# Kernel tuning notes

Measured on AMD Instinct MI355X. Metric: run time of the kernel, lower is better.

Reference implementation:

```python
import jax, jax.numpy as jnp
import numpy as np

N_POINTS = 8192
D_FEAT = 256
WEIGHT = 1.0  # self.weight
EPS = 1e-12


def _pairwise_dist(x):
    # Euclidean pairwise distances, [N, N]
    sq = jnp.sum(x * x, axis=-1)
    d2 = sq[:, None] + sq[None, :] - 2.0 * (x @ x.T)
    d2 = jnp.maximum(d2, 0.0)
    return jnp.sqrt(d2 + EPS)


def _mst_edge_weights(dist):
    # Prim's algorithm, vectorized O(N^2). The MST edge lengths are exactly
    # the death times of the H0 (dim-0) persistence diagram of the
    # Vietoris-Rips filtration (all births = 0). jit-compatible via lax.scan.
    n = dist.shape[0]
    big = jnp.asarray(1e30, dist.dtype)
    in_tree0 = jnp.zeros((n,), dtype=bool).at[0].set(True)
    mindist0 = dist[0]

    def step(carry, _):
        in_tree, mindist = carry
        masked = jnp.where(in_tree, big, mindist)
        j = jnp.argmin(masked)
        w = masked[j]                      # weight of MST edge added this step
        in_tree = in_tree.at[j].set(True)
        mindist = jnp.minimum(mindist, dist[j])
        return (in_tree, mindist), w

    _, weights = jax.lax.scan(step, (in_tree0, mindist0), None, length=n - 1)
    return weights  # [N-1] H0 death times


def _persistent_entropy(lifetimes):
    # PersistentEntropy.compute: p_i = l_i / sum(l); E = -sum p_i log p_i
    total = jnp.sum(lifetimes)
    p = lifetimes / (total + EPS)
    return -jnp.sum(p * jnp.log(p + EPS))


def setup_inputs() -> dict:
    key = jax.random.key(0)
    representations = jax.random.normal(key, (N_POINTS, D_FEAT), dtype=jnp.float32)
    return {"representations": representations}


def reference(representations):
    # PersistentHomology.compute_from_distance: VR filtration over the point
    # cloud; H0 diagram computed exactly via MST (single-linkage). Higher
    # dims (dim=1) are not produced, so the `if dim < len(diagrams)` guard
    # skips them, matching GPU PH implementations that emit H0 only.
    dist = _pairwise_dist(representations)
    deaths = _mst_edge_weights(dist)
    entropy = _persistent_entropy(deaths)
    loss = -entropy  # target_entropy is None -> maximize entropy
    return WEIGHT * loss
```

## Files before the change

kernel.cpp:

```cpp
#include <hip/hip_runtime.h>
#include <hip/hip_bf16.h>
#include <hip/hip_fp16.h>

#define NP 8192
#define DF 256
#define NROUNDS 13
#define CAND_K 48
#define NBINS 2048

typedef unsigned long long u64;
typedef unsigned int u32;
typedef unsigned short u16;
using bf16x8 = __attribute__((ext_vector_type(8))) short;
using f32x4  = __attribute__((ext_vector_type(4))) float;
using u16x8  = __attribute__((ext_vector_type(8))) u16;

__device__ __forceinline__ u16 f2bf(float f) {
  __hip_bfloat16 h = __float2bfloat16(f);
  return __builtin_bit_cast(u16, h);
}
__device__ __forceinline__ u16 f2h_bits(float f) {
  _Float16 h = (_Float16)f;
  return __builtin_bit_cast(u16, h);
}


__global__ void init_kernel(int* comp, u64* compmin, int* edgeCnt, int* nComps) {
  int i = blockIdx.x * 256 + threadIdx.x;
  if (i < NP) { comp[i] = i; compmin[i] = ~0ull; }
  if (i == 0) { *edgeCnt = 0; *nComps = NP; }
}


__global__ __launch_bounds__(64) void sq_kernel(const float* __restrict__ X, float* __restrict__ sq) {
  int i = blockIdx.x;
  float4 v = ((const float4*)(X + (size_t)i * DF))[threadIdx.x];
  float s = v.x * v.x + v.y * v.y + v.z * v.z + v.w * v.w;
#pragma unroll
  for (int off = 32; off >= 1; off >>= 1) s += __shfl_down(s, off);
  if (threadIdx.x == 0) sq[i] = s;
}


__global__ __launch_bounds__(256) void cvt_kernel(const float* __restrict__ X, u16* __restrict__ Xb) {
  int idx = (blockIdx.x * 256 + threadIdx.x) * 8;
  float4 a = ((const float4*)(X + idx))[0];
  float4 b = ((const float4*)(X + idx))[1];
  u16x8 o;
  o[0] = f2bf(a.x); o[1] = f2bf(a.y); o[2] = f2bf(a.z); o[3] = f2bf(a.w);
  o[4] = f2bf(b.x); o[5] = f2bf(b.y); o[6] = f2bf(b.z); o[7] = f2bf(b.w);
  *(u16x8*)(Xb + idx) = o;
}


template <bool PRE>
__global__ __launch_bounds__(256) void build_dist_kernel(
    const float* __restrict__ X, const u16* __restrict__ Xb,
    const float* __restrict__ sq, _Float16* __restrict__ d2) {
  __shared__ __align__(16) u16 smem[128 * 144];
  u16* At = smem;
  u16* Bt = smem + 128 * 40;
  const int t = threadIdx.x;
  const int m0 = blockIdx.y * 128, n0 = blockIdx.x * 128;
  const int wid = t >> 6, lane = t & 63;
  const int wm = wid >> 1, wn = wid & 1;
  const int lrow = lane & 15, lk = lane >> 4;
  f32x4 acc[4][4] = {};

  const int srow = t >> 1, shalf = t & 1;
  for (int k0 = 0; k0 < DF; k0 += 32) {
    u16x8 av0, av1, bv0, bv1;
    if (PRE) {
      const u16* pa = Xb + (size_t)(m0 + srow) * DF + k0 + shalf * 16;
      av0 = *(const u16x8*)pa; av1 = *(const u16x8*)(pa + 8);
      const u16* pb = Xb + (size_t)(n0 + srow) * DF + k0 + shalf * 16;
      bv0 = *(const u16x8*)pb; bv1 = *(const u16x8*)(pb + 8);
    } else {
      const float4* pa = (const float4*)(X + (size_t)(m0 + srow) * DF + k0 + shalf * 16);
      float4 a0 = pa[0], a1 = pa[1], a2 = pa[2], a3 = pa[3];
      av0[0]=f2bf(a0.x); av0[1]=f2bf(a0.y); av0[2]=f2bf(a0.z); av0[3]=f2bf(a0.w);
      av0[4]=f2bf(a1.x); av0[5]=f2bf(a1.y); av0[6]=f2bf(a1.z); av0[7]=f2bf(a1.w);
      av1[0]=f2bf(a2.x); av1[1]=f2bf(a2.y); av1[2]=f2bf(a2.z); av1[3]=f2bf(a2.w);
      av1[4]=f2bf(a3.x); av1[5]=f2bf(a3.y); av1[6]=f2bf(a3.z); av1[7]=f2bf(a3.w);
      const float4* pb = (const float4*)(X + (size_t)(n0 + srow) * DF + k0 + shalf * 16);
      float4 b0 = pb[0], b1 = pb[1], b2 = pb[2], b3 = pb[3];
      bv0[0]=f2bf(b0.x); bv0[1]=f2bf(b0.y); bv0[2]=f2bf(b0.z); bv0[3]=f2bf(b0.w);
      bv0[4]=f2bf(b1.x); bv0[5]=f2bf(b1.y); bv0[6]=f2bf(b1.z); bv0[7]=f2bf(b1.w);
      bv1[0]=f2bf(b2.x); bv1[1]=f2bf(b2.y); bv1[2]=f2bf(b2.z); bv1[3]=f2bf(b2.w);
      bv1[4]=f2bf(b3.x); bv1[5]=f2bf(b3.y); bv1[6]=f2bf(b3.z); bv1[7]=f2bf(b3.w);
    }
    __syncthreads();
    *(u16x8*)&At[srow * 40 + shalf * 16] = av0;
    *(u16x8*)&At[srow * 40 + shalf * 16 + 8] = av1;
    *(u16x8*)&Bt[srow * 40 + shalf * 16] = bv0;
    *(u16x8*)&Bt[srow * 40 + shalf * 16 + 8] = bv1;
    __syncthreads();
    bf16x8 af[4], bfr[4];
#pragma unroll
    for (int fm = 0; fm < 4; ++fm)
      af[fm] = *(const bf16x8*)&At[(wm * 64 + fm * 16 + lrow) * 40 + lk * 8];
#pragma unroll
    for (int fn = 0; fn < 4; ++fn)
      bfr[fn] = *(const bf16x8*)&Bt[(wn * 64 + fn * 16 + lrow) * 40 + lk * 8];
#pragma unroll
    for (int fm = 0; fm < 4; ++fm)
#pragma unroll
      for (int fn = 0; fn < 4; ++fn)
        acc[fm][fn] = __builtin_amdgcn_mfma_f32_16x16x32_bf16(af[fm], bfr[fn], acc[fm][fn], 0, 0, 0);
  }
  __syncthreads();

  float sqj[4];
#pragma unroll
  for (int fn = 0; fn < 4; ++fn) sqj[fn] = sq[n0 + wn * 64 + fn * 16 + lrow];
#pragma unroll
  for (int fm = 0; fm < 4; ++fm) {
#pragma unroll
    for (int r = 0; r < 4; ++r) {
      int row = wm * 64 + fm * 16 + lk * 4 + r;
      int i = m0 + row;
      float si = sq[i];
#pragma unroll
      for (int fn = 0; fn < 4; ++fn) {
        int col = wn * 64 + fn * 16 + lrow;
        float dd = si + sqj[fn] - 2.0f * acc[fm][fn][r];
        dd = fmaxf(dd, 0.0f);
        if (i == n0 + col) dd = INFINITY;
        smem[row * 144 + col] = f2h_bits(dd);
      }
    }
  }
  __syncthreads();
#pragma unroll
  for (int k = 0; k < 8; ++k) {
    int flat = k * 256 + t;
    int row = flat >> 4, cb = (flat & 15) * 8;
    *(u16x8*)&d2[(size_t)(m0 + row) * NP + n0 + cb] = *(const u16x8*)&smem[row * 144 + cb];
  }
}


__global__ __launch_bounds__(256) void topk_kernel(const _Float16* __restrict__ d2,
                                                   u64* __restrict__ candT,
                                                   u32* __restrict__ candCnt) {
  __shared__ u16 rowbuf[NP];
  __shared__ u32 hist[NBINS];
  __shared__ u32 scanw[4];
  __shared__ int swred[4];
  __shared__ int sB;
  __shared__ u32 sCnt;
  const int i = blockIdx.x;
  const int t = threadIdx.x;
  const u16* row = (const u16*)(d2 + (size_t)i * NP);
  for (int b = t; b < NBINS; b += 256) hist[b] = 0;
  if (t == 0) sCnt = 0;
  __syncthreads();
  for (int base = t * 8; base < NP; base += 2048) {
    u16x8 v = *(const u16x8*)(row + base);
    *(u16x8*)&rowbuf[base] = v;
#pragma unroll
    for (int q = 0; q < 8; ++q) atomicAdd(&hist[v[q] >> 5], 1u);
  }
  __syncthreads();
  u32 loc[8]; u32 s = 0;
#pragma unroll
  for (int q = 0; q < 8; ++q) { loc[q] = hist[t * 8 + q]; s += loc[q]; }
  u32 pre = s;
  for (int off = 1; off < 64; off <<= 1) {
    u32 o = __shfl_up(pre, off);
    if ((t & 63) >= off) pre += o;
  }
  if ((t & 63) == 63) scanw[t >> 6] = pre;
  __syncthreads();
  u32 wbase = 0;
  for (int w = 0; w < (t >> 6); ++w) wbase += scanw[w];
  u32 c = wbase + pre - s;
  int lb = -1;
#pragma unroll
  for (int q = 0; q < 8; ++q) {
    c += loc[q];
    if (c >= 1 && c <= CAND_K) lb = t * 8 + q;
  }
#pragma unroll
  for (int off = 32; off >= 1; off >>= 1) {
    int o = __shfl_down(lb, off);
    lb = lb > o ? lb : o;
  }
  if ((t & 63) == 0) swred[t >> 6] = lb;
  __syncthreads();
  if (t == 0) {
    int m = swred[0];
#pragma unroll
    for (int w = 1; w < 4; ++w) m = m > swred[w] ? m : swred[w];
    sB = m;
  }
  __syncthreads();
  const int B = sB;
  if (B >= 0) {
    for (int base = t * 8; base < NP; base += 2048) {
#pragma unroll
      for (int q = 0; q < 8; ++q) {
        u16 v = rowbuf[base + q];
        if ((int)(v >> 5) <= B) {
          u32 pos = atomicAdd(&sCnt, 1u);
          if (pos < CAND_K) {
            int j = base + q;
            int lo = i < j ? i : j;
            int hi = i ^ j ^ lo;
            candT[(size_t)pos * NP + i] = ((u64)v << 26) | ((u64)lo << 13) | (u64)hi;
          }
        }
      }
    }
  }
  __syncthreads();
  if (t == 0) {
    u32 n = sCnt;
    candCnt[i] = (n == 0 || n > CAND_K) ? 0x80000000u : n;
  }
}


__global__ __launch_bounds__(256) void round_min_kernel(
    const _Float16* __restrict__ d2, const u64* __restrict__ candT,
    const u32* __restrict__ candCnt, const int* __restrict__ comp,
    u64* __restrict__ compmin, const int* __restrict__ nComps) {
  if (*nComps == 1) return;
  __shared__ int fbl[256];
  __shared__ int fbn;
  __shared__ u64 sred[4];
  const int t = threadIdx.x;
  const int i = blockIdx.x * 256 + t;
  if (t == 0) fbn = 0;
  __syncthreads();
  const int ci = comp[i];
  u32 cc = candCnt[i];
  int n = (int)(cc & 0x7fffffffu);
  u64 best = ~0ull;
  for (int k = 0; k < n; ++k) {
    u64 key = candT[(size_t)k * NP + i];
    int lo = (int)((key >> 13) & 0x1FFF);
    int hi = (int)(key & 0x1FFF);
    int j = (lo == i) ? hi : lo;
    if (comp[j] != ci && key < best) best = key;
  }
  if (best != ~0ull && !(cc & 0x80000000u)) {
    atomicMin(&compmin[ci], best);
  } else {
    int p = atomicAdd(&fbn, 1);
    fbl[p] = i;
  }
  __syncthreads();
  for (int f = 0; f < fbn; ++f) {
    int r = fbl[f];
    int cr = comp[r];
    const u16* rowp = (const u16*)(d2 + (size_t)r * NP);
    u64 b2 = ~0ull;
    for (int base = t * 8; base < NP; base += 2048) {
      u16x8 v = *(const u16x8*)(rowp + base);
      int4 c0 = *(const int4*)(comp + base);
      int4 c1 = *(const int4*)(comp + base + 4);
      int cs[8] = {c0.x, c0.y, c0.z, c0.w, c1.x, c1.y, c1.z, c1.w};
#pragma unroll
      for (int q = 0; q < 8; ++q) {
        if (cs[q] != cr) {
          int j = base + q;
          int lo = r < j ? r : j;
          int hi = r ^ j ^ lo;
          u64 k = ((u64)v[q] << 26) | ((u64)lo << 13) | (u64)hi;
          b2 = k < b2 ? k : b2;
        }
      }
    }
#pragma unroll
    for (int off = 32; off >= 1; off >>= 1) {
      u64 o = __shfl_down(b2, off);
      b2 = b2 < o ? b2 : o;
    }
    if ((t & 63) == 0) sred[t >> 6] = b2;
    __syncthreads();
    if (t == 0) {
      b2 = sred[0];
#pragma unroll
      for (int w = 1; w < 4; ++w) b2 = b2 < sred[w] ? b2 : sred[w];
      if (b2 != ~0ull) atomicMin(&compmin[cr], b2);
    }
    __syncthreads();
  }
}


__global__ void select_kernel(const float* __restrict__ X, const float* __restrict__ sq,
                              const int* __restrict__ comp, const u64* __restrict__ compmin,
                              int* __restrict__ parent, float* __restrict__ edgeW,
                              int* __restrict__ edgeCnt, const int* __restrict__ nComps) {
  int c = blockIdx.x * blockDim.x + threadIdx.x;
  if (c >= NP) return;
  if (*nComps == 1) { parent[c] = c; return; }
  u64 m = compmin[c];
  if (m == ~0ull) { parent[c] = c; return; }
  int a = (int)((m >> 13) & 0x1FFF);
  int b = (int)(m & 0x1FFF);
  int j = (comp[a] == c) ? b : a;
  int d = comp[j];
  bool mutual = false;
  u64 md = compmin[d];
  if (md != ~0ull) {
    int a2 = (int)((md >> 13) & 0x1FFF);
    int b2 = (int)(md & 0x1FFF);
    int j2 = (comp[a2] == d) ? b2 : a2;
    mutual = (comp[j2] == c);
  }
  if (mutual && c > d) { parent[c] = d; return; }
  parent[c] = mutual ? c : d;
  const float4* pa = (const float4*)(X + (size_t)a * DF);
  const float4* pb = (const float4*)(X + (size_t)b * DF);
  float dot = 0.f;
#pragma unroll 8
  for (int k = 0; k < DF / 4; ++k) {
    float4 va = pa[k], vb = pb[k];
    dot += va.x * vb.x + va.y * vb.y + va.z * vb.z + va.w * vb.w;
  }
  float dd = sq[a] + sq[b] - 2.f * dot;
  float w = sqrtf(fmaxf(dd, 0.f) + 1e-12f);
  int idx = atomicAdd(edgeCnt, 1);
  if (idx < NP) edgeW[idx] = w;
}


__global__ __launch_bounds__(1024) void jump_relabel_kernel(
    const int* __restrict__ parent, int* __restrict__ comp,
    u64* __restrict__ compmin, int* __restrict__ nComps) {
  if (*nComps == 1) return;
  __shared__ int sp[NP];
  __shared__ unsigned char fl[NP];
  __shared__ int scnt;
  __shared__ int sch;
  const int t = threadIdx.x;
  for (int c = t; c < NP; c += 1024) { sp[c] = parent[c]; fl[c] = 0; }
  if (t == 0) { scnt = 0; sch = 0; }
  __syncthreads();
  for (int it = 0; it < NROUNDS; ++it) {
    int ch = 0;
    for (int c = t; c < NP; c += 1024) {
      int p = sp[c];
      int pp = sp[p];
      if (p != pp) { sp[c] = pp; ch = 1; }
    }
    if (ch) sch = 1;
    __syncthreads();
    if (!sch) break;
    __syncthreads();
    if (t == 0) sch = 0;
    __syncthreads();
  }
  int part = 0;
  for (int i = t; i < NP; i += 1024) {
    int nc = sp[comp[i]];
    comp[i] = nc;
    fl[nc] = 1;
  }
  __syncthreads();
  for (int c = t; c < NP; c += 1024) part += fl[c];
#pragma unroll
  for (int off = 32; off >= 1; off >>= 1) part += __shfl_down(part, off);
  if ((t & 63) == 0) atomicAdd(&scnt, part);
  for (int c = t; c < NP; c += 1024) compmin[c] = ~0ull;
  __syncthreads();
  if (t == 0) *nComps = scnt;
}


__global__ __launch_bounds__(1024) void entropy_kernel(const float* __restrict__ edgeW,
                                                       const int* __restrict__ edgeCnt,
                                                       float* __restrict__ out) {
  __shared__ float sred[16];
  __shared__ float stot;
  int ne = *edgeCnt;
  if (ne > NP) ne = NP;
  float s = 0.f;
  for (int k = threadIdx.x; k < ne; k += 1024) s += edgeW[k];
#pragma unroll
  for (int off = 32; off >= 1; off >>= 1) s += __shfl_down(s, off);
  int lane = threadIdx.x & 63, wv = threadIdx.x >> 6;
  if (lane == 0) sred[wv] = s;
  __syncthreads();
  if (threadIdx.x == 0) {
    float tt = 0.f;
#pragma unroll
    for (int w = 0; w < 16; ++w) tt += sred[w];
    stot = tt;
  }
  __syncthreads();
  float total = stot;
  float acc = 0.f;
  for (int k = threadIdx.x; k < ne; k += 1024) {
    float p = edgeW[k] / (total + 1e-12f);
    acc += p * logf(p + 1e-12f);
  }
#pragma unroll
  for (int off = 32; off >= 1; off >>= 1) acc += __shfl_down(acc, off);
  if (lane == 0) sred[wv] = acc;
  __syncthreads();
  if (threadIdx.x == 0) {
    float tt = 0.f;
#pragma unroll
    for (int w = 0; w < 16; ++w) tt += sred[w];
    out[0] = tt;
  }
}


extern "C" void kernel_launch(void* const* d_in, const int* in_sizes, int n_in,
                              void* d_out, int out_size, void* d_ws, size_t ws_size,
                              hipStream_t stream) {
  const float* X = (const float*)d_in[0];
  float* out = (float*)d_out;
  char* ws = (char*)d_ws;

  const size_t nn = (size_t)NP * NP;
  size_t off = (nn * 2 + 255) & ~(size_t)255;
  _Float16* d2 = (_Float16*)ws;
  float* sq = (float*)(ws + off);      off += (size_t)NP * 4;
  int* comp = (int*)(ws + off);        off += (size_t)NP * 4;
  u64* compmin = (u64*)(ws + off);     off += (size_t)NP * 8;
  int* parent = (int*)(ws + off);      off += (size_t)NP * 4;
  float* edgeW = (float*)(ws + off);   off += (size_t)NP * 4;
  u32* candCnt = (u32*)(ws + off);     off += (size_t)NP * 4;
  int* edgeCnt = (int*)(ws + off);     off += 64;
  int* nComps = (int*)(ws + off);      off += 64;
  off = (off + 255) & ~(size_t)255;
  u16* Xb = (u16*)(ws + off);
  u64* candT = (u64*)(ws + off);
  const bool PRE = (ws_size >= off + (size_t)NP * DF * 2);

  init_kernel<<<NP / 256, 256, 0, stream>>>(comp, compmin, edgeCnt, nComps);
  sq_kernel<<<NP, 64, 0, stream>>>(X, sq);
  if (PRE) {
    cvt_kernel<<<NP * DF / (256 * 8), 256, 0, stream>>>(X, Xb);
    build_dist_kernel<true><<<dim3(NP / 128, NP / 128), 256, 0, stream>>>(X, Xb, sq, d2);
  } else {
    build_dist_kernel<false><<<dim3(NP / 128, NP / 128), 256, 0, stream>>>(X, Xb, sq, d2);
  }
  topk_kernel<<<NP, 256, 0, stream>>>(d2, candT, candCnt);
  for (int r = 0; r < NROUNDS; ++r) {
    round_min_kernel<<<NP / 256, 256, 0, stream>>>(d2, candT, candCnt, comp, compmin, nComps);
    select_kernel<<<NP / 256, 256, 0, stream>>>(X, sq, comp, compmin, parent, edgeW, edgeCnt, nComps);
    jump_relabel_kernel<<<1, 1024, 0, stream>>>(parent, comp, compmin, nComps);
  }
  entropy_kernel<<<1, 1024, 0, stream>>>(edgeW, edgeCnt, out);
}
```

Before: 428.4 us.

## Contract graph to dense component matrix after early Boruvka rounds

Splits the Boruvka MST into two phases. After a few rounds over candidate lists, components are densely relabeled and one pass over the full distance matrix builds a component-by-component min-edge matrix (NC=512). The remaining rounds then run on that small matrix instead of rescanning rows. Fallback row scans also move out of a per-block serial loop into a separate grid-wide kernel. The design assumes at most 512 components remain after four rounds; if more remain, the dense ids overflow and the result is wrong.

```diff
diff --git a/kernel.cpp b/kernel.cpp
--- a/kernel.cpp
+++ b/kernel.cpp
@@ -4,9 +4,12 @@
 
 #define NP 8192
 #define DF 256
-#define NROUNDS 13
+#define PH1 4
+#define PH2 9
+#define NC 512
 #define CAND_K 48
 #define NBINS 2048
+#define ALLR 13
 
 typedef unsigned long long u64;
 typedef unsigned int u32;
@@ -23,11 +26,17 @@
   _Float16 h = (_Float16)f;
   return __builtin_bit_cast(u16, h);
 }
-
-
-__global__ void init_kernel(int* comp, u64* compmin, int* edgeCnt, int* nComps) {
+__device__ __forceinline__ u64 mkkey(u32 vbits, int i, int j) {
+  int lo = i < j ? i : j;
+  int hi = i ^ j ^ lo;
+  return ((u64)vbits << 26) | ((u64)lo << 13) | (u64)hi;
+}
+
+
+__global__ void init_kernel(int* comp, u64* compmin, int* edgeCnt, int* nComps, int* fbCnt) {
   int i = blockIdx.x * 256 + threadIdx.x;
   if (i < NP) { comp[i] = i; compmin[i] = ~0ull; }
+  if (blockIdx.x == 0 && threadIdx.x < 16) fbCnt[threadIdx.x] = 0;
   if (i == 0) { *edgeCnt = 0; *nComps = NP; }
 }
 
@@ -203,12 +212,7 @@
         u16 v = rowbuf[base + q];
         if ((int)(v >> 5) <= B) {
           u32 pos = atomicAdd(&sCnt, 1u);
-          if (pos < CAND_K) {
-            int j = base + q;
-            int lo = i < j ? i : j;
-            int hi = i ^ j ^ lo;
-            candT[(size_t)pos * NP + i] = ((u64)v << 26) | ((u64)lo << 13) | (u64)hi;
-          }
+          if (pos < CAND_K) candT[(size_t)pos * NP + i] = mkkey(v, i, base + q);
         }
       }
     }
@@ -221,18 +225,13 @@
 }
 
 
-__global__ __launch_bounds__(256) void round_min_kernel(
-    const _Float16* __restrict__ d2, const u64* __restrict__ candT,
-    const u32* __restrict__ candCnt, const int* __restrict__ comp,
-    u64* __restrict__ compmin, const int* __restrict__ nComps) {
+__global__ __launch_bounds__(256) void cand_min_kernel(
+    const u64* __restrict__ candT, const u32* __restrict__ candCnt,
+    const int* __restrict__ comp, u64* __restrict__ compmin,
+    const int* __restrict__ nComps, int* __restrict__ fbList,
+    int* __restrict__ fbCnt, int r) {
   if (*nComps == 1) return;
-  __shared__ int fbl[256];
-  __shared__ int fbn;
-  __shared__ u64 sred[4];
-  const int t = threadIdx.x;
-  const int i = blockIdx.x * 256 + t;
-  if (t == 0) fbn = 0;
-  __syncthreads();
+  const int i = blockIdx.x * 256 + threadIdx.x;
   const int ci = comp[i];
   u32 cc = candCnt[i];
   int n = (int)(cc & 0x7fffffffu);
@@ -247,43 +246,50 @@
   if (best != ~0ull && !(cc & 0x80000000u)) {
     atomicMin(&compmin[ci], best);
   } else {
-    int p = atomicAdd(&fbn, 1);
-    fbl[p] = i;
-  }
-  __syncthreads();
-  for (int f = 0; f < fbn; ++f) {
-    int r = fbl[f];
-    int cr = comp[r];
-    const u16* rowp = (const u16*)(d2 + (size_t)r * NP);
-    u64 b2 = ~0ull;
+    int p = atomicAdd(&fbCnt[r], 1);
+    fbList[p] = i;
+  }
+}
+
+
+__global__ __launch_bounds__(256) void fb_kernel(
+    const _Float16* __restrict__ d2, const int* __restrict__ comp,
+    u64* __restrict__ compmin, const int* __restrict__ fbList,
+    const int* __restrict__ fbCnt, int r, const int* __restrict__ nComps) {
+  if (*nComps == 1) return;
+  __shared__ u64 sred[4];
+  const int t = threadIdx.x;
+  const int n = fbCnt[r];
+  for (int idx = blockIdx.x; idx < n; idx += gridDim.x) {
+    const int i = fbList[idx];
+    const int ci = comp[i];
+    const u16* row = (const u16*)(d2 + (size_t)i * NP);
+    u64 best = ~0ull;
     for (int base = t * 8; base < NP; base += 2048) {
-      u16x8 v = *(const u16x8*)(rowp + base);
+      u16x8 v = *(const u16x8*)(row + base);
       int4 c0 = *(const int4*)(comp + base);
       int4 c1 = *(const int4*)(comp + base + 4);
       int cs[8] = {c0.x, c0.y, c0.z, c0.w, c1.x, c1.y, c1.z, c1.w};
 #pragma unroll
       for (int q = 0; q < 8; ++q) {
-        if (cs[q] != cr) {
-          int j = base + q;
-          int lo = r < j ? r : j;
-          int hi = r ^ j ^ lo;
-          u64 k = ((u64)v[q] << 26) | ((u64)lo << 13) | (u64)hi;
-          b2 = k < b2 ? k : b2;
+        if (cs[q] != ci) {
+          u64 k = mkkey(v[q], i, base + q);
+          best = k < best ? k : best;
         }
       }
     }
 #pragma unroll
     for (int off = 32; off >= 1; off >>= 1) {
-      u64 o = __shfl_down(b2, off);
-      b2 = b2 < o ? b2 : o;
-    }
-    if ((t & 63) == 0) sred[t >> 6] = b2;
+      u64 o = __shfl_down(best, off);
+      best = best < o ? best : o;
+    }
+    if ((t & 63) == 0) sred[t >> 6] = best;
     __syncthreads();
     if (t == 0) {
-      b2 = sred[0];
-#pragma unroll
-      for (int w = 1; w < 4; ++w) b2 = b2 < sred[w] ? b2 : sred[w];
-      if (b2 != ~0ull) atomicMin(&compmin[cr], b2);
+      best = sred[0];
+#pragma unroll
+      for (int w = 1; w < 4; ++w) best = best < sred[w] ? best : sred[w];
+      if (best != ~0ull) atomicMin(&compmin[ci], best);
     }
     __syncthreads();
   }
@@ -328,19 +334,24 @@
 }
 
 
+template <bool DENSE>
 __global__ __launch_bounds__(1024) void jump_relabel_kernel(
     const int* __restrict__ parent, int* __restrict__ comp,
-    u64* __restrict__ compmin, int* __restrict__ nComps) {
+    u64* __restrict__ compmin, int* __restrict__ nComps,
+    u16* __restrict__ dcomp, int* __restrict__ comp2, int* __restrict__ parent2,
+    u64* __restrict__ compmin2, int* __restrict__ ncDense) {
   if (*nComps == 1) return;
   __shared__ int sp[NP];
-  __shared__ unsigned char fl[NP];
+  __shared__ u16 did[NP];
+  __shared__ int swsum[16];
   __shared__ int scnt;
   __shared__ int sch;
   const int t = threadIdx.x;
-  for (int c = t; c < NP; c += 1024) { sp[c] = parent[c]; fl[c] = 0; }
+  const int lane = t & 63, wv = t >> 6;
+  for (int c = t; c < NP; c += 1024) { sp[c] = parent[c]; did[c] = 0; }
   if (t == 0) { scnt = 0; sch = 0; }
   __syncthreads();
-  for (int it = 0; it < NROUNDS; ++it) {
+  for (int it = 0; it < 13; ++it) {
     int ch = 0;
     for (int c = t; c < NP; c += 1024) {
       int p = sp[c];
@@ -354,18 +365,183 @@
     if (t == 0) sch = 0;
     __syncthreads();
   }
-  int part = 0;
   for (int i = t; i < NP; i += 1024) {
     int nc = sp[comp[i]];
     comp[i] = nc;
-    fl[nc] = 1;
-  }
-  __syncthreads();
-  for (int c = t; c < NP; c += 1024) part += fl[c];
+    did[nc] = 1;
+  }
+  __syncthreads();
+  if constexpr (!DENSE) {
+    int part = 0;
+    for (int c = t; c < NP; c += 1024) part += did[c];
+#pragma unroll
+    for (int off = 32; off >= 1; off >>= 1) part += __shfl_down(part, off);
+    if (lane == 0) atomicAdd(&scnt, part);
+    for (int c = t; c < NP; c += 1024) compmin[c] = ~0ull;
+    __syncthreads();
+    if (t == 0) *nComps = scnt;
+  } else {
+    int f[8]; int s = 0;
+#pragma unroll
+    for (int q = 0; q < 8; ++q) { f[q] = did[t * 8 + q]; s += f[q]; }
+    int incl = s;
+    for (int off = 1; off < 64; off <<= 1) {
+      int o = __shfl_up(incl, off);
+      if (lane >= off) incl += o;
+    }
+    if (lane == 63) swsum[wv] = incl;
+    __syncthreads();
+    int wbase = 0;
+    for (int w = 0; w < wv; ++w) wbase += swsum[w];
+    int e = wbase + incl - s;
+#pragma unroll
+    for (int q = 0; q < 8; ++q) {
+      if (f[q]) { did[t * 8 + q] = (u16)e; ++e; }
+    }
+    __syncthreads();
+    for (int i = t; i < NP; i += 1024) dcomp[i] = did[comp[i]];
+    if (t < NC) { comp2[t] = t; parent2[t] = t; compmin2[t] = ~0ull; }
+    if (t == 0) {
+      int total = 0;
+#pragma unroll
+      for (int w = 0; w < 16; ++w) total += swsum[w];
+      *nComps = total;
+      *ncDense = total;
+    }
+  }
+}
+
+
+__global__ __launch_bounds__(256) void minit_kernel(u64* __restrict__ M) {
+  int idx = (blockIdx.x * 256 + threadIdx.x) * 4;
+#pragma unroll
+  for (int q = 0; q < 4; ++q) M[idx + q] = ~0ull;
+}
+
+
+__global__ __launch_bounds__(256) void contract_kernel(
+    const _Float16* __restrict__ d2, const u16* __restrict__ dcomp,
+    u64* __restrict__ M) {
+  __shared__ u32 table[NC];
+  const int i = blockIdx.x;
+  const int t = threadIdx.x;
+  for (int b = t; b < NC; b += 256) table[b] = ~0u;
+  __syncthreads();
+  const int ci = dcomp[i];
+  const u16* row = (const u16*)(d2 + (size_t)i * NP);
+  for (int base = t * 8; base < NP; base += 2048) {
+    u16x8 v = *(const u16x8*)(row + base);
+    u16x8 cj = *(const u16x8*)(dcomp + base);
+#pragma unroll
+    for (int q = 0; q < 8; ++q) {
+      if (cj[q] != ci) {
+        u32 k32 = ((u32)v[q] << 13) | (u32)(base + q);
+        atomicMin(&table[cj[q]], k32);
+      }
+    }
+  }
+  __syncthreads();
+  for (int b = t; b < NC; b += 256) {
+    u32 k32 = table[b];
+    if (k32 != ~0u) {
+      u64 key = mkkey(k32 >> 13, i, (int)(k32 & 0x1FFF));
+      u64* addr = &M[(size_t)ci * NC + b];
+      if (key < *addr) atomicMin(addr, key);
+    }
+  }
+}
+
+
+__global__ __launch_bounds__(64) void rmin2_kernel(const u64* __restrict__ M,
+                                                   const int* __restrict__ comp2,
+                                                   u64* __restrict__ compmin2,
+                                                   const int* __restrict__ nComps) {
+  if (*nComps == 1) return;
+  const int a = blockIdx.x;
+  const int t = threadIdx.x;
+  const int ca = comp2[a];
+  u64 best = ~0ull;
+  for (int b = t; b < NC; b += 64) {
+    u64 k = M[(size_t)a * NC + b];
+    if (k != ~0ull && comp2[b] != ca && k < best) best = k;
+  }
+#pragma unroll
+  for (int off = 32; off >= 1; off >>= 1) {
+    u64 o = __shfl_down(best, off);
+    best = best < o ? best : o;
+  }
+  if (t == 0 && best != ~0ull) atomicMin(&compmin2[ca], best);
+}
+
+
+__global__ void select2_kernel(const float* __restrict__ X, const float* __restrict__ sq,
+                               const u16* __restrict__ dcomp, const int* __restrict__ comp2,
+                               const u64* __restrict__ compmin2, int* __restrict__ parent2,
+                               float* __restrict__ edgeW, int* __restrict__ edgeCnt,
+                               const int* __restrict__ nComps) {
+  int c = blockIdx.x * blockDim.x + threadIdx.x;
+  if (c >= NC) return;
+  if (*nComps == 1) { parent2[c] = c; return; }
+  u64 m = compmin2[c];
+  if (m == ~0ull) { parent2[c] = c; return; }
+  int a = (int)((m >> 13) & 0x1FFF);
+  int b = (int)(m & 0x1FFF);
+  int j = (comp2[dcomp[a]] == c) ? b : a;
+  int d = comp2[dcomp[j]];
+  bool mutual = false;
+  u64 md = compmin2[d];
+  if (md != ~0ull) {
+    int a2 = (int)((md >> 13) & 0x1FFF);
+    int b2 = (int)(md & 0x1FFF);
+    int j2 = (comp2[dcomp[a2]] == d) ? b2 : a2;
+    mutual = (comp2[dcomp[j2]] == c);
+  }
+  if (mutual && c > d) { parent2[c] = d; return; }
+  parent2[c] = mutual ? c : d;
+  const float4* pa = (const float4*)(X + (size_t)a * DF);
+  const float4* pb = (const float4*)(X + (size_t)b * DF);
+  float dot = 0.f;
+#pragma unroll 8
+  for (int k = 0; k < DF / 4; ++k) {
+    float4 va = pa[k], vb = pb[k];
+    dot += va.x * vb.x + va.y * vb.y + va.z * vb.z + va.w * vb.w;
+  }
+  float dd = sq[a] + sq[b] - 2.f * dot;
+  float w = sqrtf(fmaxf(dd, 0.f) + 1e-12f);
+  int idx = atomicAdd(edgeCnt, 1);
+  if (idx < NP) edgeW[idx] = w;
+}
+
+
+__global__ __launch_bounds__(NC) void jump2_kernel(const int* __restrict__ parent2,
+                                                   int* __restrict__ comp2,
+                                                   u64* __restrict__ compmin2,
+                                                   int* __restrict__ nComps,
+                                                   const int* __restrict__ ncDense) {
+  if (*nComps == 1) return;
+  __shared__ int sp[NC];
+  __shared__ u16 fl[NC];
+  __shared__ int scnt;
+  const int t = threadIdx.x;
+  sp[t] = parent2[t];
+  fl[t] = 0;
+  if (t == 0) scnt = 0;
+  __syncthreads();
+#pragma unroll
+  for (int it = 0; it < 9; ++it) {
+    sp[t] = sp[sp[t]];
+    __syncthreads();
+  }
+  int nd = *ncDense;
+  int nc2 = sp[comp2[t]];
+  comp2[t] = nc2;
+  if (t < nd) fl[nc2] = 1;
+  __syncthreads();
+  int part = fl[t];
 #pragma unroll
   for (int off = 32; off >= 1; off >>= 1) part += __shfl_down(part, off);
   if ((t & 63) == 0) atomicAdd(&scnt, part);
-  for (int c = t; c < NP; c += 1024) compmin[c] = ~0ull;
+  compmin2[t] = ~0ull;
   __syncthreads();
   if (t == 0) *nComps = scnt;
 }
@@ -427,14 +603,23 @@
   int* parent = (int*)(ws + off);      off += (size_t)NP * 4;
   float* edgeW = (float*)(ws + off);   off += (size_t)NP * 4;
   u32* candCnt = (u32*)(ws + off);     off += (size_t)NP * 4;
+  int* fbList = (int*)(ws + off);      off += (size_t)NP * 4;
+  u16* dcomp = (u16*)(ws + off);       off += (size_t)NP * 2;
+  int* comp2 = (int*)(ws + off);       off += (size_t)NC * 4;
+  int* parent2 = (int*)(ws + off);     off += (size_t)NC * 4;
+  u64* compmin2 = (u64*)(ws + off);    off += (size_t)NC * 8;
   int* edgeCnt = (int*)(ws + off);     off += 64;
   int* nComps = (int*)(ws + off);      off += 64;
+  int* ncDense = (int*)(ws + off);     off += 64;
+  int* fbCnt = (int*)(ws + off);       off += 64;
   off = (off + 255) & ~(size_t)255;
   u16* Xb = (u16*)(ws + off);
   u64* candT = (u64*)(ws + off);
+  u64* M = (u64*)(ws + off);
   const bool PRE = (ws_size >= off + (size_t)NP * DF * 2);
-
-  init_kernel<<<NP / 256, 256, 0, stream>>>(comp, compmin, edgeCnt, nComps);
+  const bool useM = (ws_size >= off + (size_t)NC * NC * 8);
+
+  init_kernel<<<NP / 256, 256, 0, stream>>>(comp, compmin, edgeCnt, nComps, fbCnt);
   sq_kernel<<<NP, 64, 0, stream>>>(X, sq);
   if (PRE) {
     cvt_kernel<<<NP * DF / (256 * 8), 256, 0, stream>>>(X, Xb);
@@ -443,10 +628,33 @@
     build_dist_kernel<false><<<dim3(NP / 128, NP / 128), 256, 0, stream>>>(X, Xb, sq, d2);
   }
   topk_kernel<<<NP, 256, 0, stream>>>(d2, candT, candCnt);
-  for (int r = 0; r < NROUNDS; ++r) {
-    round_min_kernel<<<NP / 256, 256, 0, stream>>>(d2, candT, candCnt, comp, compmin, nComps);
-    select_kernel<<<NP / 256, 256, 0, stream>>>(X, sq, comp, compmin, parent, edgeW, edgeCnt, nComps);
-    jump_relabel_kernel<<<1, 1024, 0, stream>>>(parent, comp, compmin, nComps);
-  }
+
+  const int p1 = useM ? PH1 : ALLR;
+  for (int r = 0; r < p1; ++r) {
+    cand_min_kernel<<<NP / 256, 256, 0, stream>>>(candT, candCnt, comp, compmin, nComps,
+                                                  fbList, fbCnt, r);
+    fb_kernel<<<128, 256, 0, stream>>>(d2, comp, compmin, fbList, fbCnt, r, nComps);
+    select_kernel<<<NP / 256, 256, 0, stream>>>(X, sq, comp, compmin, parent, edgeW,
+                                                edgeCnt, nComps);
+    if (useM && r == p1 - 1) {
+      jump_relabel_kernel<true><<<1, 1024, 0, stream>>>(parent, comp, compmin, nComps,
+                                                        dcomp, comp2, parent2, compmin2, ncDense);
+    } else {
+      jump_relabel_kernel<false><<<1, 1024, 0, stream>>>(parent, comp, compmin, nComps,
+                                                         dcomp, comp2, parent2, compmin2, ncDense);
+    }
+  }
+
+  if (useM) {
+    minit_kernel<<<NC * NC / (256 * 4), 256, 0, stream>>>(M);
+    contract_kernel<<<NP, 256, 0, stream>>>(d2, dcomp, M);
+    for (int r = 0; r < PH2; ++r) {
+      rmin2_kernel<<<NC, 64, 0, stream>>>(M, comp2, compmin2, nComps);
+      select2_kernel<<<NC / 256, 256, 0, stream>>>(X, sq, dcomp, comp2, compmin2, parent2,
+                                                   edgeW, edgeCnt, nComps);
+      jump2_kernel<<<1, NC, 0, stream>>>(parent2, comp2, compmin2, nComps, ncDense);
+    }
+  }
+
   entropy_kernel<<<1, 1024, 0, stream>>>(edgeW, edgeCnt, out);
 }
```

Measured after the change: 459.1 us. +7.2%, slower.
